# Kernel tuning notes

Hardware: AMD Instinct MI355X
Metric: run time of the kernel (lower is better)

The kernel has to match this reference:

```python
import jax, jax.numpy as jnp
import numpy as np
from jax import lax

B, L, F, D_MODEL = 4, 256, 80, 2048
ED, N, DT_RANK, K, NL = 4096, 16, 2, 4, 6  # d_inner, d_state, dt_rank, d_conv, n_layers


def setup_inputs():
    key = jax.random.key(0)
    ks = jax.random.split(key, 12)
    rn = lambda k, shp, s=0.02: jax.random.normal(k, shp, dtype=jnp.float32) * s
    return {
        "x": jax.random.normal(ks[0], (B, F, L), dtype=jnp.float32),
        "W_emb": rn(ks[1], (F, D_MODEL)),
        "b_emb": jnp.zeros((D_MODEL,), jnp.float32),
        "norm_w": jnp.ones((NL, D_MODEL), jnp.float32),
        "W_in": rn(ks[2], (NL, D_MODEL, 2 * ED)),
        "b_in": jnp.zeros((NL, 2 * ED), jnp.float32),
        "conv_w": rn(ks[3], (NL, ED, K), 0.1),
        "conv_b": jnp.zeros((NL, ED), jnp.float32),
        "W_x": rn(ks[4], (NL, ED, DT_RANK + 2 * N)),
        "W_dt": rn(ks[5], (NL, DT_RANK, ED), 0.1),
        "b_dt": jnp.full((NL, ED), -4.0, jnp.float32),
        "A_log": jnp.tile(jnp.log(jnp.arange(1, N + 1, dtype=jnp.float32))[None, None, :], (NL, ED, 1)),
        "Dp": jnp.ones((NL, ED), jnp.float32),
        "W_out": rn(ks[6], (NL, ED, D_MODEL)),
        "b_out": jnp.zeros((NL, D_MODEL), jnp.float32),
        "W_f": rn(ks[7], (D_MODEL, 1024)),
        "b_f": jnp.zeros((1024,), jnp.float32),
        "W_h1": rn(ks[8], (1024, 512), 0.05),
        "b_h1": jnp.zeros((512,), jnp.float32),
        "W_h2": rn(ks[9], (512, 256), 0.05),
        "b_h2": jnp.zeros((256,), jnp.float32),
        "W_h3": rn(ks[10], (256, 1), 0.05),
        "b_h3": jnp.zeros((1,), jnp.float32),
    }


def _rmsnorm(x, w, eps=1e-5):
    return x * lax.rsqrt(jnp.mean(x * x, axis=-1, keepdims=True) + eps) * w


def _mamba_block(u, W_in, b_in, conv_w, conv_b, W_x, W_dt, b_dt, A_log, Dp, W_out, b_out):
    xz = u @ W_in + b_in                        # (B,L,2*ED)
    xp, z = jnp.split(xz, 2, axis=-1)
    # causal depthwise conv over time, kernel K
    xc = lax.conv_general_dilated(
        xp.transpose(0, 2, 1), conv_w[:, None, :],
        window_strides=(1,), padding=[(K - 1, 0)],
        feature_group_count=ED,
        dimension_numbers=("NCH", "OIH", "NCH")).transpose(0, 2, 1) + conv_b
    xa = jax.nn.silu(xc)                        # (B,L,ED)
    dbc = xa @ W_x                              # (B,L,dt_rank+2N)
    dt = jax.nn.softplus(dbc[..., :DT_RANK] @ W_dt + b_dt)   # (B,L,ED)
    Bm = dbc[..., DT_RANK:DT_RANK + N]
    Cm = dbc[..., DT_RANK + N:]
    A = -jnp.exp(A_log)                         # (ED,N), negative

    def step(h, inp):
        xa_t, dt_t, B_t, C_t = inp
        h = jnp.exp(dt_t[:, :, None] * A) * h + (dt_t * xa_t)[:, :, None] * B_t[:, None, :]
        return h, jnp.einsum("ben,bn->be", h, C_t)

    step = jax.checkpoint(step)
    h0 = jnp.zeros((xa.shape[0], ED, N), xa.dtype)
    _, ys = lax.scan(step, h0, (xa.transpose(1, 0, 2), dt.transpose(1, 0, 2),
                                Bm.transpose(1, 0, 2), Cm.transpose(1, 0, 2)))
    y = ys.transpose(1, 0, 2) + Dp * xa
    y = y * jax.nn.silu(z)
    return y @ W_out + b_out


def reference(x, W_emb, b_emb, norm_w, W_in, b_in, conv_w, conv_b, W_x, W_dt, b_dt, A_log, Dp, W_out, b_out, W_f, b_f, W_h1, b_h1, W_h2, b_h2, W_h3, b_h3):
    h = x.transpose(0, 2, 1) @ W_emb + b_emb    # (B,L,D_MODEL)
    for i in range(NL):
        h = h + _mamba_block(_rmsnorm(h, norm_w[i]), W_in[i], b_in[i], conv_w[i], conv_b[i],
                             W_x[i], W_dt[i], b_dt[i], A_log[i], Dp[i], W_out[i], b_out[i])
    f = h[:, -1] @ W_f + b_f                    # (B,1024)
    g = jax.nn.silu(f @ W_h1 + b_h1)
    g = g @ W_h2 + b_h2
    g = jnp.where(g > 0, g, 0.01 * g)           # LeakyReLU(0.01)
    return jax.nn.sigmoid(g @ W_h3 + b_h3)      # (B,1)
```

## Files before the change

kernel.cpp:

```cpp
#include <hip/hip_runtime.h>
#include <hip/hip_bf16.h>
#include <math.h>

#define D_MODEL 2048
#define EDIM    4096
#define NSTATE  16
#define LSEQ    256
#define BATCH   4
#define NLAYER  6
#define FDIM    80

typedef __attribute__((ext_vector_type(8))) short bf16x8;
typedef __attribute__((ext_vector_type(4))) float f32x4;

__device__ __forceinline__ float silu_f(float x) { return x / (1.f + __expf(-x)); }

__device__ __forceinline__ float softplus_f(float v) {
  return (v > 20.f) ? v : __logf(1.f + __expf(v));
}

__device__ __forceinline__ unsigned short f2bf(float f) {
  unsigned u = __float_as_uint(f);
  unsigned r = u + 0x7fffu + ((u >> 16) & 1u);
  return (unsigned short)(r >> 16);
}

__device__ __forceinline__ void gload_lds16(const void* g, void* l) {
  __builtin_amdgcn_global_load_lds(
      (const __attribute__((address_space(1))) unsigned int*)g,
      (__attribute__((address_space(3))) unsigned int*)l, 16, 0, 0);
}

__global__ __launch_bounds__(256) void embed_kernel(
    const float* __restrict__ x, const float* __restrict__ W,
    const float* __restrict__ bias, float* __restrict__ h)
{
  int col = blockIdx.x * 256 + threadIdx.x;
  int row = blockIdx.y;
  int b = row >> 8, l = row & 255;
  const float* xp = x + (size_t)b * FDIM * LSEQ + l;
  float acc = bias[col];
  #pragma unroll 8
  for (int f = 0; f < FDIM; ++f)
    acc = fmaf(xp[(size_t)f * LSEQ], W[(size_t)f * D_MODEL + col], acc);
  h[(size_t)row * D_MODEL + col] = acc;
}

__global__ __launch_bounds__(256) void rmsnorm_kernel(
    const float* __restrict__ h, const float* __restrict__ w, unsigned short* __restrict__ u)
{
  int row = blockIdx.x;
  const float* hr = h + (size_t)row * D_MODEL;
  float s = 0.f;
  for (int i = threadIdx.x; i < D_MODEL; i += 256) { float v = hr[i]; s = fmaf(v, v, s); }
  #pragma unroll
  for (int o = 32; o > 0; o >>= 1) s += __shfl_down(s, o);
  __shared__ float red[4];
  int lane = threadIdx.x & 63, wid = threadIdx.x >> 6;
  if (lane == 0) red[wid] = s;
  __syncthreads();
  float total = red[0] + red[1] + red[2] + red[3];
  float scale = rsqrtf(total * (1.f / D_MODEL) + 1e-5f);
  unsigned short* ur = u + (size_t)row * D_MODEL;
  for (int i = threadIdx.x; i < D_MODEL; i += 256) ur[i] = f2bf(hr[i] * scale * w[i]);
}

__global__ __launch_bounds__(256) void wtrans_kernel(
    const float* __restrict__ W, unsigned short* __restrict__ WT, int K, int N)
{
  __shared__ float t[64][65];
  const int k0 = blockIdx.y * 64, n0 = blockIdx.x * 64;
  const int tc = (threadIdx.x & 15) << 2;
  const int tr = threadIdx.x >> 4;
  #pragma unroll
  for (int i = 0; i < 4; ++i) {
    int r = tr + (i << 4);
    float4 v = *(const float4*)(W + (size_t)(k0 + r) * N + n0 + tc);
    t[r][tc + 0] = v.x; t[r][tc + 1] = v.y; t[r][tc + 2] = v.z; t[r][tc + 3] = v.w;
  }
  __syncthreads();
  #pragma unroll
  for (int i = 0; i < 4; ++i) {
    int rr = tr + (i << 4);
    ushort4 o;
    o.x = f2bf(t[tc + 0][rr]);
    o.y = f2bf(t[tc + 1][rr]);
    o.z = f2bf(t[tc + 2][rr]);
    o.w = f2bf(t[tc + 3][rr]);
    *(ushort4*)(WT + (size_t)(n0 + rr) * K + k0 + tc) = o;
  }
}

__global__ __launch_bounds__(256) void wxt_kernel(
    const float* __restrict__ Wx, float* __restrict__ WxT)
{
  const int e = blockIdx.x * 256 + threadIdx.x;
  const int j = blockIdx.y;
  const int l = blockIdx.z;
  WxT[((size_t)l * 34 + j) * EDIM + e] = Wx[(size_t)l * EDIM * 34 + (size_t)e * 34 + j];
}

template<int BN>
__global__ __launch_bounds__(256) void gemm_bf16(
    const unsigned short* __restrict__ A, int lda,
    const unsigned short* __restrict__ BT, int ldb,
    const float* __restrict__ bias,
    const float* resid, int ldr,
    float* __restrict__ C, int ldc, int K)
{
  constexpr int BM = 128;
  constexpr int FN = BN / 32;
  __shared__ unsigned short As[2][BM * 32];
  __shared__ unsigned short Bs[2][BN * 32];
  const int tid  = threadIdx.x;
  const int wave = tid >> 6;
  const int lane = tid & 63;

  const int nwg = gridDim.x * gridDim.y;
  const int cpx = nwg >> 3;
  int flat = blockIdx.y * gridDim.x + blockIdx.x;
  flat = (flat & 7) * cpx + (flat >> 3);
  const int bm = (flat / gridDim.x) * BM;
  const int bn = (flat % gridDim.x) * BN;

  const int wr = (wave >> 1) * 64;
  const int wc = (wave & 1) * (BN / 2);
  const int srow = lane >> 2;
  const int scol = (lane & 3) * 8;

  auto stage = [&](int buf, int k0) {
    #pragma unroll
    for (int i = 0; i < BM / 64; ++i) {
      int c = wave + i * 4;
      gload_lds16(A + (size_t)(bm + c * 16 + srow) * lda + k0 + scol, &As[buf][c * 512]);
    }
    #pragma unroll
    for (int i = 0; i < BN / 64; ++i) {
      int c = wave + i * 4;
      gload_lds16(BT + (size_t)(bn + c * 16 + srow) * ldb + k0 + scol, &Bs[buf][c * 512]);
    }
  };

  f32x4 acc[4][FN];
  #pragma unroll
  for (int m = 0; m < 4; ++m)
    #pragma unroll
    for (int n = 0; n < FN; ++n)
      acc[m][n] = (f32x4){0.f, 0.f, 0.f, 0.f};

  stage(0, 0);
  const int nk = K >> 5;
  for (int t = 0; t < nk; ++t) {
    const int cur = t & 1;
    __syncthreads();
    if (t + 1 < nk) stage(cur ^ 1, (t + 1) << 5);
    bf16x8 af[4], bfr[FN];
    #pragma unroll
    for (int m = 0; m < 4; ++m)
      af[m] = *(const bf16x8*)&As[cur][(wr + m * 16 + (lane & 15)) * 32 + (lane >> 4) * 8];
    #pragma unroll
    for (int n = 0; n < FN; ++n)
      bfr[n] = *(const bf16x8*)&Bs[cur][(wc + n * 16 + (lane & 15)) * 32 + (lane >> 4) * 8];
    #pragma unroll
    for (int m = 0; m < 4; ++m)
      #pragma unroll
      for (int n = 0; n < FN; ++n)
        acc[m][n] = __builtin_amdgcn_mfma_f32_16x16x32_bf16(af[m], bfr[n], acc[m][n], 0, 0, 0);
  }

  const int rbase = (lane >> 4) * 4;
  const int cbase = lane & 15;
  #pragma unroll
  for (int m = 0; m < 4; ++m) {
    #pragma unroll
    for (int n = 0; n < FN; ++n) {
      const int col = bn + wc + n * 16 + cbase;
      const float bv = bias[col];
      #pragma unroll
      for (int r = 0; r < 4; ++r) {
        const int row = bm + wr + m * 16 + rbase + r;
        float v = acc[m][n][r] + bv;
        if (resid) v += resid[(size_t)row * ldr + col];
        C[(size_t)row * ldc + col] = v;
      }
    }
  }
}

__global__ __launch_bounds__(256) void conv_dbc_kernel(
    const float* __restrict__ xz, const float* __restrict__ cw,
    const float* __restrict__ cb, const float* __restrict__ WxT,
    float* __restrict__ xa, float* __restrict__ dbc)
{
  const int row = blockIdx.x;
  const int l = row & (LSEQ - 1);
  const int tid = threadIdx.x;
  float a[16];
  const float* base_row = xz + (size_t)row * 8192;
  #pragma unroll
  for (int k = 0; k < 16; ++k) {
    const int e = k * 256 + tid;
    float4 w = *(const float4*)(cw + (size_t)e * 4);
    const float* base = base_row + e;
    float v = cb[e];
    v = fmaf(w.w, base[0], v);
    if (l >= 1) v = fmaf(w.z, base[-8192], v);
    if (l >= 2) v = fmaf(w.y, base[-2 * 8192], v);
    if (l >= 3) v = fmaf(w.x, base[-3 * 8192], v);
    v = silu_f(v);
    a[k] = v;
    xa[(size_t)row * EDIM + e] = v;
  }
  __shared__ float red[34][4];
  const int lane = tid & 63, wid = tid >> 6;
  #pragma unroll
  for (int j = 0; j < 34; ++j) {
    const float* wr = WxT + (size_t)j * EDIM + tid;
    float s = 0.f;
    #pragma unroll
    for (int k = 0; k < 16; ++k)
      s = fmaf(a[k], wr[k * 256], s);
    #pragma unroll
    for (int o = 32; o > 0; o >>= 1) s += __shfl_down(s, o);
    if (lane == 0) red[j][wid] = s;
  }
  __syncthreads();
  if (tid < 34)
    dbc[(size_t)row * 34 + tid] = red[tid][0] + red[tid][1] + red[tid][2] + red[tid][3];
}

struct ScanIn { float x[4], z[4], d0[4], d1[4], B0[4], B1[4], C0[4], C1[4]; };

__device__ __forceinline__ void scan_load(
    ScanIn& s, const float* xap, const float* zp, const float* dp, int t0, int g)
{
  #pragma unroll
  for (int u = 0; u < 4; ++u) {
    const int t = t0 + u;
    s.x[u] = xap[(size_t)t * EDIM];
    s.z[u] = zp[(size_t)t * 8192];
    const float* dr = dp + (size_t)t * 34;
    s.d0[u] = dr[0];           s.d1[u] = dr[1];
    s.B0[u] = dr[2 + 2 * g];   s.B1[u] = dr[3 + 2 * g];
    s.C0[u] = dr[18 + 2 * g];  s.C1[u] = dr[19 + 2 * g];
  }
}

__device__ __forceinline__ void scan_step(
    const ScanIn& s, float& h0, float& h1,
    float w0, float w1, float bde, float Aa0, float Aa1, float dpe,
    int g, unsigned short* yp, int t0)
{
  #pragma unroll
  for (int u = 0; u < 4; ++u) {
    float v = fmaf(s.d1[u], w1, fmaf(s.d0[u], w0, bde));
    float dta = softplus_f(v);
    float dtxa = dta * s.x[u];
    h0 = fmaf(__expf(dta * Aa0), h0, dtxa * s.B0[u]);
    h1 = fmaf(__expf(dta * Aa1), h1, dtxa * s.B1[u]);
    float part = fmaf(h0, s.C0[u], h1 * s.C1[u]);
    part += __shfl_xor(part, 8);
    part += __shfl_xor(part, 16);
    part += __shfl_xor(part, 32);
    if (g == 0) {
      float yv = fmaf(dpe, s.x[u], part);
      yp[(size_t)(t0 + u) * EDIM] = f2bf(yv * silu_f(s.z[u]));
    }
  }
}

__global__ __launch_bounds__(256) void scan_kernel(
    const float* __restrict__ xz, const float* __restrict__ xa,
    const float* __restrict__ dbc,
    const float* __restrict__ Wdt, const float* __restrict__ bdt,
    const float* __restrict__ Alog, const float* __restrict__ Dpp,
    unsigned short* __restrict__ ybf)
{
  const int b = blockIdx.x >> 7;
  const int chunk = blockIdx.x & 127;
  const int wave = threadIdx.x >> 6;
  const int lane = threadIdx.x & 63;
  const int ch = lane & 7;
  const int g = lane >> 3;
  const int e = chunk * 32 + wave * 8 + ch;

  const float w0 = Wdt[e], w1 = Wdt[EDIM + e], bde = bdt[e];
  const float Aa0 = -__expf(Alog[(size_t)e * 16 + g * 2]);
  const float Aa1 = -__expf(Alog[(size_t)e * 16 + g * 2 + 1]);
  const float dpe = Dpp[e];
  float h0 = 0.f, h1 = 0.f;

  const float* xap = xa + (size_t)(b << 8) * EDIM + e;
  const float* zp  = xz + (size_t)(b << 8) * 8192 + EDIM + e;
  const float* dp  = dbc + (size_t)(b << 8) * 34;
  unsigned short* yp = ybf + (size_t)(b << 8) * EDIM + e;

  ScanIn sa, sb;
  scan_load(sa, xap, zp, dp, 0, g);
  for (int t0 = 0; t0 < LSEQ; t0 += 8) {
    scan_load(sb, xap, zp, dp, t0 + 4, g);
    scan_step(sa, h0, h1, w0, w1, bde, Aa0, Aa1, dpe, g, yp, t0);
    if (t0 + 8 < LSEQ) scan_load(sa, xap, zp, dp, t0 + 8, g);
    scan_step(sb, h0, h1, w0, w1, bde, Aa0, Aa1, dpe, g, yp, t0 + 4);
  }
}

template<int KS>
__global__ __launch_bounds__(256) void head_gemm_part(
    const float* __restrict__ in, int in_stride,
    const float* __restrict__ W, int N,
    float* __restrict__ part)
{
  const int j = blockIdx.x * 256 + threadIdx.x;
  const int b = blockIdx.y;
  const int s = blockIdx.z;
  const int k0 = s * KS;
  __shared__ float sIn[KS];
  if (threadIdx.x < KS) sIn[threadIdx.x] = in[(size_t)b * in_stride + k0 + threadIdx.x];
  __syncthreads();
  float acc = 0.f;
  #pragma unroll 8
  for (int k = 0; k < KS; ++k)
    acc = fmaf(sIn[k], W[(size_t)(k0 + k) * N + j], acc);
  part[((size_t)s * gridDim.y + b) * N + j] = acc;
}

__global__ __launch_bounds__(256) void head_reduce(
    const float* __restrict__ part, const float* __restrict__ bias,
    float* __restrict__ outp, int N, int S, int act)
{
  const int j = blockIdx.x * 256 + threadIdx.x;
  const int b = blockIdx.y;
  const int B = gridDim.y;
  float acc = bias[j];
  for (int s = 0; s < S; ++s)
    acc += part[((size_t)s * B + b) * N + j];
  if (act == 1) acc = silu_f(acc);
  else if (act == 2) acc = (acc > 0.f) ? acc : 0.01f * acc;
  outp[(size_t)b * N + j] = acc;
}

__global__ __launch_bounds__(256) void head_final_kernel(
    const float* __restrict__ g2, const float* __restrict__ W,
    const float* __restrict__ bb, float* __restrict__ out)
{
  int b_idx = threadIdx.x >> 6;
  int lane = threadIdx.x & 63;
  float s = 0.f;
  #pragma unroll
  for (int i = 0; i < 4; ++i) {
    int k = lane + i * 64;
    s = fmaf(g2[b_idx * 256 + k], W[k], s);
  }
  #pragma unroll
  for (int o = 32; o > 0; o >>= 1) s += __shfl_down(s, o);
  if (lane == 0) out[b_idx] = 1.f / (1.f + __expf(-(s + bb[0])));
}

extern "C" void kernel_launch(void* const* d_in, const int* in_sizes, int n_in,
                              void* d_out, int out_size, void* d_ws, size_t ws_size,
                              hipStream_t stream)
{
  const float* x      = (const float*)d_in[0];
  const float* W_emb  = (const float*)d_in[1];
  const float* b_emb  = (const float*)d_in[2];
  const float* norm_w = (const float*)d_in[3];
  const float* W_in   = (const float*)d_in[4];
  const float* b_in   = (const float*)d_in[5];
  const float* conv_w = (const float*)d_in[6];
  const float* conv_b = (const float*)d_in[7];
  const float* W_x    = (const float*)d_in[8];
  const float* W_dt   = (const float*)d_in[9];
  const float* b_dt   = (const float*)d_in[10];
  const float* A_log  = (const float*)d_in[11];
  const float* Dp     = (const float*)d_in[12];
  const float* W_out  = (const float*)d_in[13];
  const float* b_out  = (const float*)d_in[14];
  const float* W_f    = (const float*)d_in[15];
  const float* b_f    = (const float*)d_in[16];
  const float* W_h1   = (const float*)d_in[17];
  const float* b_h1   = (const float*)d_in[18];
  const float* W_h2   = (const float*)d_in[19];
  const float* b_h2   = (const float*)d_in[20];
  const float* W_h3   = (const float*)d_in[21];
  const float* b_h3   = (const float*)d_in[22];
  float* out = (float*)d_out;

  char* ws = (char*)d_ws;
  float*          hA  = (float*)ws;                 ws += (size_t)1024 * 2048 * 4;
  float*          hB  = (float*)ws;                 ws += (size_t)1024 * 2048 * 4;
  unsigned short* ubf = (unsigned short*)ws;        ws += (size_t)1024 * 2048 * 2;
  float*          xz  = (float*)ws;                 ws += (size_t)1024 * 8192 * 4;
  float*          xa  = (float*)ws;                 ws += (size_t)1024 * 4096 * 4;
  float*          dbc = (float*)ws;                 ws += (size_t)1024 * 40 * 4;
  unsigned short* ybf = (unsigned short*)ws;        ws += (size_t)1024 * 4096 * 2;
  unsigned short* WT  = (unsigned short*)ws;        ws += (size_t)8192 * 2048 * 2;
  float*          WxT = (float*)ws;                 ws += (size_t)NLAYER * 34 * EDIM * 4;
  float*          part= (float*)ws;                 ws += (size_t)16 * 4 * 1024 * 4;
  float*          fb  = (float*)ws;                 ws += 4096 * 4;
  float*          g1b = (float*)ws;                 ws += 2048 * 4;
  float*          g2b = (float*)ws;                 ws += 1024 * 4;

  embed_kernel<<<dim3(D_MODEL / 256, 1024), 256, 0, stream>>>(x, W_emb, b_emb, hA);
  wxt_kernel<<<dim3(EDIM / 256, 34, NLAYER), 256, 0, stream>>>(W_x, WxT);

  float* hin = hA;
  float* hout = hB;
  for (int i = 0; i < NLAYER; ++i) {
    const float* Wi  = W_in  + (size_t)i * 2048 * 8192;
    const float* bi  = b_in  + (size_t)i * 8192;
    const float* cwi = conv_w + (size_t)i * 4096 * 4;
    const float* cbi = conv_b + (size_t)i * 4096;
    const float* Wdti= W_dt  + (size_t)i * 2 * 4096;
    const float* bdti= b_dt  + (size_t)i * 4096;
    const float* Ali = A_log + (size_t)i * 4096 * 16;
    const float* Dpi = Dp    + (size_t)i * 4096;
    const float* Woi = W_out + (size_t)i * 4096 * 2048;
    const float* boi = b_out + (size_t)i * 2048;
    const float* nwi = norm_w + (size_t)i * 2048;

    rmsnorm_kernel<<<1024, 256, 0, stream>>>(hin, nwi, ubf);
    wtrans_kernel<<<dim3(8192 / 64, 2048 / 64), 256, 0, stream>>>(Wi, WT, 2048, 8192);
    gemm_bf16<128><<<dim3(8192 / 128, 1024 / 128), 256, 0, stream>>>(
        ubf, 2048, WT, 2048, bi, nullptr, 0, xz, 8192, 2048);
    conv_dbc_kernel<<<1024, 256, 0, stream>>>(
        xz, cwi, cbi, WxT + (size_t)i * 34 * EDIM, xa, dbc);
    scan_kernel<<<512, 256, 0, stream>>>(xz, xa, dbc, Wdti, bdti, Ali, Dpi, ybf);
    wtrans_kernel<<<dim3(2048 / 64, 4096 / 64), 256, 0, stream>>>(Woi, WT, 4096, 2048);
    gemm_bf16<64><<<dim3(2048 / 64, 1024 / 128), 256, 0, stream>>>(
        ybf, 4096, WT, 4096, boi, hin, 2048, hout, 2048, 4096);
    float* tmp = hin; hin = hout; hout = tmp;
  }

  head_gemm_part<128><<<dim3(1024 / 256, BATCH, 16), 256, 0, stream>>>(
      hin + (size_t)255 * 2048, 256 * 2048, W_f, 1024, part);
  head_reduce<<<dim3(1024 / 256, BATCH), 256, 0, stream>>>(part, b_f, fb, 1024, 16, 0);
  head_gemm_part<128><<<dim3(512 / 256, BATCH, 8), 256, 0, stream>>>(
      fb, 1024, W_h1, 512, part);
  head_reduce<<<dim3(512 / 256, BATCH), 256, 0, stream>>>(part, b_h1, g1b, 512, 8, 1);
  head_gemm_part<128><<<dim3(256 / 256, BATCH, 4), 256, 0, stream>>>(
      g1b, 512, W_h2, 256, part);
  head_reduce<<<dim3(256 / 256, BATCH), 256, 0, stream>>>(part, b_h2, g2b, 256, 4, 2);
  head_final_kernel<<<1, 256, 0, stream>>>(g2b, W_h3, b_h3, out);
}
```

Before: 1.799 ms.

## Split conv and x_proj, compute x_proj with bf16 MFMA GEMM

The fused conv+dbc kernel, which did per-row FP32 dot products against the transposed W_x, is split into an elementwise conv+SiLU kernel that also writes a bf16 copy of xa, followed by the bf16 MFMA GEMM. W_x is pre-transposed into bf16 padded to 64 columns, and dbc gets a stride of 64. The GEMM launches only 8 workgroups (1x8 grid) with K=4096, so parallelism is very low. Rounding xa and W_x to bf16 also reduces the precision of dt, B and C.

```diff
diff --git a/kernel.cpp b/kernel.cpp
--- a/kernel.cpp
+++ b/kernel.cpp
@@ -91,20 +91,21 @@
   }
 }
 
-__global__ __launch_bounds__(256) void wxt_kernel(
-    const float* __restrict__ Wx, float* __restrict__ WxT)
+__global__ __launch_bounds__(256) void wxtb_kernel(
+    const float* __restrict__ Wx, unsigned short* __restrict__ WxTb)
 {
   const int e = blockIdx.x * 256 + threadIdx.x;
   const int j = blockIdx.y;
   const int l = blockIdx.z;
-  WxT[((size_t)l * 34 + j) * EDIM + e] = Wx[(size_t)l * EDIM * 34 + (size_t)e * 34 + j];
+  float v = (j < 34) ? Wx[(size_t)l * EDIM * 34 + (size_t)e * 34 + j] : 0.f;
+  WxTb[((size_t)l * 64 + j) * EDIM + e] = f2bf(v);
 }
 
 template<int BN>
 __global__ __launch_bounds__(256) void gemm_bf16(
     const unsigned short* __restrict__ A, int lda,
     const unsigned short* __restrict__ BT, int ldb,
-    const float* __restrict__ bias,
+    const float* bias,
     const float* resid, int ldr,
     float* __restrict__ C, int ldc, int K)
 {
@@ -175,7 +176,7 @@
     #pragma unroll
     for (int n = 0; n < FN; ++n) {
       const int col = bn + wc + n * 16 + cbase;
-      const float bv = bias[col];
+      const float bv = bias ? bias[col] : 0.f;
       #pragma unroll
       for (int r = 0; r < 4; ++r) {
         const int row = bm + wr + m * 16 + rbase + r;
@@ -187,46 +188,25 @@
   }
 }
 
-__global__ __launch_bounds__(256) void conv_dbc_kernel(
+__global__ __launch_bounds__(256) void conv_silu_kernel(
     const float* __restrict__ xz, const float* __restrict__ cw,
-    const float* __restrict__ cb, const float* __restrict__ WxT,
-    float* __restrict__ xa, float* __restrict__ dbc)
-{
-  const int row = blockIdx.x;
-  const int l = row & (LSEQ - 1);
-  const int tid = threadIdx.x;
-  float a[16];
-  const float* base_row = xz + (size_t)row * 8192;
-  #pragma unroll
-  for (int k = 0; k < 16; ++k) {
-    const int e = k * 256 + tid;
-    float4 w = *(const float4*)(cw + (size_t)e * 4);
-    const float* base = base_row + e;
-    float v = cb[e];
-    v = fmaf(w.w, base[0], v);
-    if (l >= 1) v = fmaf(w.z, base[-8192], v);
-    if (l >= 2) v = fmaf(w.y, base[-2 * 8192], v);
-    if (l >= 3) v = fmaf(w.x, base[-3 * 8192], v);
-    v = silu_f(v);
-    a[k] = v;
-    xa[(size_t)row * EDIM + e] = v;
-  }
-  __shared__ float red[34][4];
-  const int lane = tid & 63, wid = tid >> 6;
-  #pragma unroll
-  for (int j = 0; j < 34; ++j) {
-    const float* wr = WxT + (size_t)j * EDIM + tid;
-    float s = 0.f;
-    #pragma unroll
-    for (int k = 0; k < 16; ++k)
-      s = fmaf(a[k], wr[k * 256], s);
-    #pragma unroll
-    for (int o = 32; o > 0; o >>= 1) s += __shfl_down(s, o);
-    if (lane == 0) red[j][wid] = s;
-  }
-  __syncthreads();
-  if (tid < 34)
-    dbc[(size_t)row * 34 + tid] = red[tid][0] + red[tid][1] + red[tid][2] + red[tid][3];
+    const float* __restrict__ cb, float* __restrict__ xa,
+    unsigned short* __restrict__ xab)
+{
+  int idx = blockIdx.x * 256 + threadIdx.x;
+  int e = idx & (EDIM - 1);
+  int row = idx >> 12;
+  int l = row & (LSEQ - 1);
+  float4 w = *(const float4*)(cw + (size_t)e * 4);
+  const float* base = xz + (size_t)row * 8192 + e;
+  float v = cb[e];
+  v = fmaf(w.w, base[0], v);
+  if (l >= 1) v = fmaf(w.z, base[-8192], v);
+  if (l >= 2) v = fmaf(w.y, base[-2 * 8192], v);
+  if (l >= 3) v = fmaf(w.x, base[-3 * 8192], v);
+  v = silu_f(v);
+  xa[idx] = v;
+  xab[idx] = f2bf(v);
 }
 
 struct ScanIn { float x[4], z[4], d0[4], d1[4], B0[4], B1[4], C0[4], C1[4]; };
@@ -239,7 +219,7 @@
     const int t = t0 + u;
     s.x[u] = xap[(size_t)t * EDIM];
     s.z[u] = zp[(size_t)t * 8192];
-    const float* dr = dp + (size_t)t * 34;
+    const float* dr = dp + (size_t)t * 64;
     s.d0[u] = dr[0];           s.d1[u] = dr[1];
     s.B0[u] = dr[2 + 2 * g];   s.B1[u] = dr[3 + 2 * g];
     s.C0[u] = dr[18 + 2 * g];  s.C1[u] = dr[19 + 2 * g];
@@ -292,7 +272,7 @@
 
   const float* xap = xa + (size_t)(b << 8) * EDIM + e;
   const float* zp  = xz + (size_t)(b << 8) * 8192 + EDIM + e;
-  const float* dp  = dbc + (size_t)(b << 8) * 34;
+  const float* dp  = dbc + (size_t)(b << 8) * 64;
   unsigned short* yp = ybf + (size_t)(b << 8) * EDIM + e;
 
   ScanIn sa, sb;
@@ -392,17 +372,18 @@
   unsigned short* ubf = (unsigned short*)ws;        ws += (size_t)1024 * 2048 * 2;
   float*          xz  = (float*)ws;                 ws += (size_t)1024 * 8192 * 4;
   float*          xa  = (float*)ws;                 ws += (size_t)1024 * 4096 * 4;
-  float*          dbc = (float*)ws;                 ws += (size_t)1024 * 40 * 4;
+  unsigned short* xab = (unsigned short*)ws;        ws += (size_t)1024 * 4096 * 2;
+  float*          dbc = (float*)ws;                 ws += (size_t)1024 * 64 * 4;
   unsigned short* ybf = (unsigned short*)ws;        ws += (size_t)1024 * 4096 * 2;
   unsigned short* WT  = (unsigned short*)ws;        ws += (size_t)8192 * 2048 * 2;
-  float*          WxT = (float*)ws;                 ws += (size_t)NLAYER * 34 * EDIM * 4;
+  unsigned short* WxTb= (unsigned short*)ws;        ws += (size_t)NLAYER * 64 * EDIM * 2;
   float*          part= (float*)ws;                 ws += (size_t)16 * 4 * 1024 * 4;
   float*          fb  = (float*)ws;                 ws += 4096 * 4;
   float*          g1b = (float*)ws;                 ws += 2048 * 4;
   float*          g2b = (float*)ws;                 ws += 1024 * 4;
 
   embed_kernel<<<dim3(D_MODEL / 256, 1024), 256, 0, stream>>>(x, W_emb, b_emb, hA);
-  wxt_kernel<<<dim3(EDIM / 256, 34, NLAYER), 256, 0, stream>>>(W_x, WxT);
+  wxtb_kernel<<<dim3(EDIM / 256, 64, NLAYER), 256, 0, stream>>>(W_x, WxTb);
 
   float* hin = hA;
   float* hout = hB;
@@ -423,8 +404,9 @@
     wtrans_kernel<<<dim3(8192 / 64, 2048 / 64), 256, 0, stream>>>(Wi, WT, 2048, 8192);
     gemm_bf16<128><<<dim3(8192 / 128, 1024 / 128), 256, 0, stream>>>(
         ubf, 2048, WT, 2048, bi, nullptr, 0, xz, 8192, 2048);
-    conv_dbc_kernel<<<1024, 256, 0, stream>>>(
-        xz, cwi, cbi, WxT + (size_t)i * 34 * EDIM, xa, dbc);
+    conv_silu_kernel<<<(1024 * 4096) / 256, 256, 0, stream>>>(xz, cwi, cbi, xa, xab);
+    gemm_bf16<64><<<dim3(1, 1024 / 128), 256, 0, stream>>>(
+        xab, 4096, WxTb + (size_t)i * 64 * EDIM, 4096, nullptr, nullptr, 0, dbc, 64, 4096);
     scan_kernel<<<512, 256, 0, stream>>>(xz, xa, dbc, Wdti, bdti, Ali, Dpi, ybf);
     wtrans_kernel<<<dim3(2048 / 64, 4096 / 64), 256, 0, stream>>>(Woi, WT, 4096, 2048);
     gemm_bf16<64><<<dim3(2048 / 64, 1024 / 128), 256, 0, stream>>>(
```

After: 2.076 ms. 15.4% more time.

## Transpose scan inputs to time-major bf16 layout for vectorized scan loads

Applied to the files above, without the earlier changes.

The conv kernel now writes its activations as bf16 and dbc transposed per batch, and a new transpose kernel converts xa and z into time-contiguous bf16 arrays. The scan then loads 8 timesteps per vector load and processes 8-step groups instead of doing strided per-step scalar loads. This targets the scan's latency-bound strided memory accesses. It adds an extra transpose kernel and its global traffic, and it lowers the precision of x and z to bf16 inside the scan.

```diff
diff --git a/kernel.cpp b/kernel.cpp
--- a/kernel.cpp
+++ b/kernel.cpp
@@ -23,6 +23,10 @@
   unsigned u = __float_as_uint(f);
   unsigned r = u + 0x7fffu + ((u >> 16) & 1u);
   return (unsigned short)(r >> 16);
+}
+
+__device__ __forceinline__ float bf2f(unsigned short u) {
+  return __uint_as_float((unsigned)u << 16);
 }
 
 __device__ __forceinline__ void gload_lds16(const void* g, void* l) {
@@ -104,7 +108,7 @@
 __global__ __launch_bounds__(256) void gemm_bf16(
     const unsigned short* __restrict__ A, int lda,
     const unsigned short* __restrict__ BT, int ldb,
-    const float* __restrict__ bias,
+    const float* bias,
     const float* resid, int ldr,
     float* __restrict__ C, int ldc, int K)
 {
@@ -175,7 +179,7 @@
     #pragma unroll
     for (int n = 0; n < FN; ++n) {
       const int col = bn + wc + n * 16 + cbase;
-      const float bv = bias[col];
+      const float bv = bias ? bias[col] : 0.f;
       #pragma unroll
       for (int r = 0; r < 4; ++r) {
         const int row = bm + wr + m * 16 + rbase + r;
@@ -190,10 +194,11 @@
 __global__ __launch_bounds__(256) void conv_dbc_kernel(
     const float* __restrict__ xz, const float* __restrict__ cw,
     const float* __restrict__ cb, const float* __restrict__ WxT,
-    float* __restrict__ xa, float* __restrict__ dbc)
+    unsigned short* __restrict__ xab, float* __restrict__ dbcT)
 {
   const int row = blockIdx.x;
   const int l = row & (LSEQ - 1);
+  const int b = row >> 8;
   const int tid = threadIdx.x;
   float a[16];
   const float* base_row = xz + (size_t)row * 8192;
@@ -209,7 +214,7 @@
     if (l >= 3) v = fmaf(w.x, base[-3 * 8192], v);
     v = silu_f(v);
     a[k] = v;
-    xa[(size_t)row * EDIM + e] = v;
+    xab[(size_t)row * EDIM + e] = f2bf(v);
   }
   __shared__ float red[34][4];
   const int lane = tid & 63, wid = tid >> 6;
@@ -226,33 +231,72 @@
   }
   __syncthreads();
   if (tid < 34)
-    dbc[(size_t)row * 34 + tid] = red[tid][0] + red[tid][1] + red[tid][2] + red[tid][3];
-}
-
-struct ScanIn { float x[4], z[4], d0[4], d1[4], B0[4], B1[4], C0[4], C1[4]; };
-
-__device__ __forceinline__ void scan_load(
-    ScanIn& s, const float* xap, const float* zp, const float* dp, int t0, int g)
-{
-  #pragma unroll
-  for (int u = 0; u < 4; ++u) {
-    const int t = t0 + u;
-    s.x[u] = xap[(size_t)t * EDIM];
-    s.z[u] = zp[(size_t)t * 8192];
-    const float* dr = dp + (size_t)t * 34;
-    s.d0[u] = dr[0];           s.d1[u] = dr[1];
-    s.B0[u] = dr[2 + 2 * g];   s.B1[u] = dr[3 + 2 * g];
-    s.C0[u] = dr[18 + 2 * g];  s.C1[u] = dr[19 + 2 * g];
-  }
-}
-
-__device__ __forceinline__ void scan_step(
-    const ScanIn& s, float& h0, float& h1,
+    dbcT[((size_t)b * 34 + tid) * 256 + l] =
+        red[tid][0] + red[tid][1] + red[tid][2] + red[tid][3];
+}
+
+__global__ __launch_bounds__(256) void tmajor_kernel(
+    const unsigned short* __restrict__ xab, const float* __restrict__ xz,
+    unsigned short* __restrict__ xT, unsigned short* __restrict__ zT)
+{
+  __shared__ unsigned short tx[64][72];
+  __shared__ unsigned short tz[64][72];
+  const int e0 = blockIdx.x * 64;
+  const int t0 = blockIdx.y * 64;
+  const int b  = blockIdx.z;
+  const int c  = threadIdx.x & 63;
+  const int r4 = threadIdx.x >> 6;
+  #pragma unroll
+  for (int i = 0; i < 16; ++i) {
+    int t = r4 + i * 4;
+    int row = (b << 8) + t0 + t;
+    tx[t][c] = xab[(size_t)row * EDIM + e0 + c];
+    tz[t][c] = f2bf(xz[(size_t)row * 8192 + EDIM + e0 + c]);
+  }
+  __syncthreads();
+  #pragma unroll
+  for (int i = 0; i < 16; ++i) {
+    int ee = r4 + i * 4;
+    xT[((size_t)b * EDIM + e0 + ee) * 256 + t0 + c] = tx[c][ee];
+    zT[((size_t)b * EDIM + e0 + ee) * 256 + t0 + c] = tz[c][ee];
+  }
+}
+
+struct ScanIn8 { float x[8], z[8], d0[8], d1[8], B0[8], B1[8], C0[8], C1[8]; };
+
+__device__ __forceinline__ void scan_load8(
+    ScanIn8& s, const unsigned short* xTp, const unsigned short* zTp,
+    const float* dp, int t0, int g)
+{
+  bf16x8 xv = *(const bf16x8*)&xTp[t0];
+  bf16x8 zv = *(const bf16x8*)&zTp[t0];
+  #pragma unroll
+  for (int u = 0; u < 8; ++u) {
+    s.x[u] = bf2f((unsigned short)xv[u]);
+    s.z[u] = bf2f((unsigned short)zv[u]);
+  }
+  const float* r;
+  r = dp + t0;                     *(float4*)&s.d0[0] = *(const float4*)&r[0];
+                                   *(float4*)&s.d0[4] = *(const float4*)&r[4];
+  r = dp + 256 + t0;               *(float4*)&s.d1[0] = *(const float4*)&r[0];
+                                   *(float4*)&s.d1[4] = *(const float4*)&r[4];
+  r = dp + (2 + 2 * g) * 256 + t0; *(float4*)&s.B0[0] = *(const float4*)&r[0];
+                                   *(float4*)&s.B0[4] = *(const float4*)&r[4];
+  r = dp + (3 + 2 * g) * 256 + t0; *(float4*)&s.B1[0] = *(const float4*)&r[0];
+                                   *(float4*)&s.B1[4] = *(const float4*)&r[4];
+  r = dp + (18 + 2 * g) * 256 + t0; *(float4*)&s.C0[0] = *(const float4*)&r[0];
+                                    *(float4*)&s.C0[4] = *(const float4*)&r[4];
+  r = dp + (19 + 2 * g) * 256 + t0; *(float4*)&s.C1[0] = *(const float4*)&r[0];
+                                    *(float4*)&s.C1[4] = *(const float4*)&r[4];
+}
+
+__device__ __forceinline__ void scan_step8(
+    const ScanIn8& s, float& h0, float& h1,
     float w0, float w1, float bde, float Aa0, float Aa1, float dpe,
     int g, unsigned short* yp, int t0)
 {
   #pragma unroll
-  for (int u = 0; u < 4; ++u) {
+  for (int u = 0; u < 8; ++u) {
     float v = fmaf(s.d1[u], w1, fmaf(s.d0[u], w0, bde));
     float dta = softplus_f(v);
     float dtxa = dta * s.x[u];
@@ -270,8 +314,8 @@
 }
 
 __global__ __launch_bounds__(256) void scan_kernel(
-    const float* __restrict__ xz, const float* __restrict__ xa,
-    const float* __restrict__ dbc,
+    const unsigned short* __restrict__ xT, const unsigned short* __restrict__ zT,
+    const float* __restrict__ dbcT,
     const float* __restrict__ Wdt, const float* __restrict__ bdt,
     const float* __restrict__ Alog, const float* __restrict__ Dpp,
     unsigned short* __restrict__ ybf)
@@ -290,18 +334,18 @@
   const float dpe = Dpp[e];
   float h0 = 0.f, h1 = 0.f;
 
-  const float* xap = xa + (size_t)(b << 8) * EDIM + e;
-  const float* zp  = xz + (size_t)(b << 8) * 8192 + EDIM + e;
-  const float* dp  = dbc + (size_t)(b << 8) * 34;
+  const unsigned short* xTp = xT + ((size_t)b * EDIM + e) * 256;
+  const unsigned short* zTp = zT + ((size_t)b * EDIM + e) * 256;
+  const float* dp = dbcT + (size_t)b * 34 * 256;
   unsigned short* yp = ybf + (size_t)(b << 8) * EDIM + e;
 
-  ScanIn sa, sb;
-  scan_load(sa, xap, zp, dp, 0, g);
-  for (int t0 = 0; t0 < LSEQ; t0 += 8) {
-    scan_load(sb, xap, zp, dp, t0 + 4, g);
-    scan_step(sa, h0, h1, w0, w1, bde, Aa0, Aa1, dpe, g, yp, t0);
-    if (t0 + 8 < LSEQ) scan_load(sa, xap, zp, dp, t0 + 8, g);
-    scan_step(sb, h0, h1, w0, w1, bde, Aa0, Aa1, dpe, g, yp, t0 + 4);
+  ScanIn8 sa, sb;
+  scan_load8(sa, xTp, zTp, dp, 0, g);
+  for (int t0 = 0; t0 < LSEQ; t0 += 16) {
+    scan_load8(sb, xTp, zTp, dp, t0 + 8, g);
+    scan_step8(sa, h0, h1, w0, w1, bde, Aa0, Aa1, dpe, g, yp, t0);
+    if (t0 + 16 < LSEQ) scan_load8(sa, xTp, zTp, dp, t0 + 16, g);
+    scan_step8(sb, h0, h1, w0, w1, bde, Aa0, Aa1, dpe, g, yp, t0 + 8);
   }
 }
 
@@ -391,8 +435,10 @@
   float*          hB  = (float*)ws;                 ws += (size_t)1024 * 2048 * 4;
   unsigned short* ubf = (unsigned short*)ws;        ws += (size_t)1024 * 2048 * 2;
   float*          xz  = (float*)ws;                 ws += (size_t)1024 * 8192 * 4;
-  float*          xa  = (float*)ws;                 ws += (size_t)1024 * 4096 * 4;
-  float*          dbc = (float*)ws;                 ws += (size_t)1024 * 40 * 4;
+  unsigned short* xab = (unsigned short*)ws;        ws += (size_t)1024 * 4096 * 2;
+  unsigned short* xT  = (unsigned short*)ws;        ws += (size_t)1024 * 4096 * 2;
+  unsigned short* zT  = (unsigned short*)ws;        ws += (size_t)1024 * 4096 * 2;
+  float*          dbcT= (float*)ws;                 ws += (size_t)4 * 34 * 256 * 4;
   unsigned short* ybf = (unsigned short*)ws;        ws += (size_t)1024 * 4096 * 2;
   unsigned short* WT  = (unsigned short*)ws;        ws += (size_t)8192 * 2048 * 2;
   float*          WxT = (float*)ws;                 ws += (size_t)NLAYER * 34 * EDIM * 4;
@@ -424,8 +470,9 @@
     gemm_bf16<128><<<dim3(8192 / 128, 1024 / 128), 256, 0, stream>>>(
         ubf, 2048, WT, 2048, bi, nullptr, 0, xz, 8192, 2048);
     conv_dbc_kernel<<<1024, 256, 0, stream>>>(
-        xz, cwi, cbi, WxT + (size_t)i * 34 * EDIM, xa, dbc);
-    scan_kernel<<<512, 256, 0, stream>>>(xz, xa, dbc, Wdti, bdti, Ali, Dpi, ybf);
+        xz, cwi, cbi, WxT + (size_t)i * 34 * EDIM, xab, dbcT);
+    tmajor_kernel<<<dim3(EDIM / 64, LSEQ / 64, BATCH), 256, 0, stream>>>(xab, xz, xT, zT);
+    scan_kernel<<<512, 256, 0, stream>>>(xT, zT, dbcT, Wdti, bdti, Ali, Dpi, ybf);
     wtrans_kernel<<<dim3(2048 / 64, 4096 / 64), 256, 0, stream>>>(Woi, WT, 4096, 2048);
     gemm_bf16<64><<<dim3(2048 / 64, 1024 / 128), 256, 0, stream>>>(
         ybf, 4096, WT, 4096, boi, hin, 2048, hout, 2048, 4096);
```

After: 1.841 ms. 1.02x slower.

## Stage scan inputs in LDS and store xa as bf16

Applied to the files above, without the earlier changes.

The conv kernel now writes its silu activation as bf16 instead of fp32, halving that buffer's traffic. The scan kernel bulk-loads its per-chunk x, z, dt and B/C slices for the whole sequence into shared memory with vectorized coalesced loads, storing most of it as bf16, then runs the recurrence from LDS. This replaces strided per-timestep global loads inside the sequential loop. It adds a bulk preload phase and lowers the precision of x, z, B and C inside the scan. The gemm bias argument also becomes nullable.

```diff
diff --git a/kernel.cpp b/kernel.cpp
--- a/kernel.cpp
+++ b/kernel.cpp
@@ -23,6 +23,10 @@
   unsigned u = __float_as_uint(f);
   unsigned r = u + 0x7fffu + ((u >> 16) & 1u);
   return (unsigned short)(r >> 16);
+}
+
+__device__ __forceinline__ float bf2f(unsigned short u) {
+  return __uint_as_float((unsigned)u << 16);
 }
 
 __device__ __forceinline__ void gload_lds16(const void* g, void* l) {
@@ -104,7 +108,7 @@
 __global__ __launch_bounds__(256) void gemm_bf16(
     const unsigned short* __restrict__ A, int lda,
     const unsigned short* __restrict__ BT, int ldb,
-    const float* __restrict__ bias,
+    const float* bias,
     const float* resid, int ldr,
     float* __restrict__ C, int ldc, int K)
 {
@@ -175,7 +179,7 @@
     #pragma unroll
     for (int n = 0; n < FN; ++n) {
       const int col = bn + wc + n * 16 + cbase;
-      const float bv = bias[col];
+      const float bv = bias ? bias[col] : 0.f;
       #pragma unroll
       for (int r = 0; r < 4; ++r) {
         const int row = bm + wr + m * 16 + rbase + r;
@@ -190,7 +194,7 @@
 __global__ __launch_bounds__(256) void conv_dbc_kernel(
     const float* __restrict__ xz, const float* __restrict__ cw,
     const float* __restrict__ cb, const float* __restrict__ WxT,
-    float* __restrict__ xa, float* __restrict__ dbc)
+    unsigned short* __restrict__ xab, float* __restrict__ dbc)
 {
   const int row = blockIdx.x;
   const int l = row & (LSEQ - 1);
@@ -209,7 +213,7 @@
     if (l >= 3) v = fmaf(w.x, base[-3 * 8192], v);
     v = silu_f(v);
     a[k] = v;
-    xa[(size_t)row * EDIM + e] = v;
+    xab[(size_t)row * EDIM + e] = f2bf(v);
   }
   __shared__ float red[34][4];
   const int lane = tid & 63, wid = tid >> 6;
@@ -230,21 +234,6 @@
 }
 
 struct ScanIn { float x[4], z[4], d0[4], d1[4], B0[4], B1[4], C0[4], C1[4]; };
-
-__device__ __forceinline__ void scan_load(
-    ScanIn& s, const float* xap, const float* zp, const float* dp, int t0, int g)
-{
-  #pragma unroll
-  for (int u = 0; u < 4; ++u) {
-    const int t = t0 + u;
-    s.x[u] = xap[(size_t)t * EDIM];
-    s.z[u] = zp[(size_t)t * 8192];
-    const float* dr = dp + (size_t)t * 34;
-    s.d0[u] = dr[0];           s.d1[u] = dr[1];
-    s.B0[u] = dr[2 + 2 * g];   s.B1[u] = dr[3 + 2 * g];
-    s.C0[u] = dr[18 + 2 * g];  s.C1[u] = dr[19 + 2 * g];
-  }
-}
 
 __device__ __forceinline__ void scan_step(
     const ScanIn& s, float& h0, float& h1,
@@ -270,37 +259,81 @@
 }
 
 __global__ __launch_bounds__(256) void scan_kernel(
-    const float* __restrict__ xz, const float* __restrict__ xa,
+    const unsigned short* __restrict__ xab, const float* __restrict__ xz,
     const float* __restrict__ dbc,
     const float* __restrict__ Wdt, const float* __restrict__ bdt,
     const float* __restrict__ Alog, const float* __restrict__ Dpp,
     unsigned short* __restrict__ ybf)
 {
+  __shared__ unsigned short sx[256 * 32];
+  __shared__ unsigned short sz[256 * 32];
+  __shared__ float          sd01[256 * 2];
+  __shared__ unsigned short sBC[256 * 32];
+
+  const int tid = threadIdx.x;
   const int b = blockIdx.x >> 7;
   const int chunk = blockIdx.x & 127;
-  const int wave = threadIdx.x >> 6;
-  const int lane = threadIdx.x & 63;
+  const int wave = tid >> 6;
+  const int lane = tid & 63;
   const int ch = lane & 7;
   const int g = lane >> 3;
-  const int e = chunk * 32 + wave * 8 + ch;
+  const int we = wave * 8 + ch;
+  const int e = chunk * 32 + we;
+
+  const unsigned short* xsrc = xab + (size_t)(b << 8) * EDIM + chunk * 32;
+  const float* zsrc = xz + (size_t)(b << 8) * 8192 + EDIM + chunk * 32;
+  const float* dsrc = dbc + (size_t)(b << 8) * 34;
+  #pragma unroll
+  for (int i = 0; i < 8; ++i) {
+    int idx = i * 256 + tid;
+    int t = idx >> 3, q = idx & 7;
+    *(ushort4*)&sx[t * 32 + q * 4] = *(const ushort4*)&xsrc[(size_t)t * EDIM + q * 4];
+    float4 v = *(const float4*)&zsrc[(size_t)t * 8192 + q * 4];
+    ushort4 o; o.x = f2bf(v.x); o.y = f2bf(v.y); o.z = f2bf(v.z); o.w = f2bf(v.w);
+    *(ushort4*)&sz[t * 32 + q * 4] = o;
+  }
+  {
+    float2 v = *(const float2*)&dsrc[(size_t)tid * 34];
+    *(float2*)&sd01[tid * 2] = v;
+  }
+  #pragma unroll
+  for (int i = 0; i < 16; ++i) {
+    int idx = i * 256 + tid;
+    int t = idx >> 4, q = idx & 15;
+    float2 v = *(const float2*)&dsrc[(size_t)t * 34 + 2 + q * 2];
+    ushort2 o; o.x = f2bf(v.x); o.y = f2bf(v.y);
+    *(ushort2*)&sBC[t * 32 + q * 2] = o;
+  }
+  __syncthreads();
 
   const float w0 = Wdt[e], w1 = Wdt[EDIM + e], bde = bdt[e];
   const float Aa0 = -__expf(Alog[(size_t)e * 16 + g * 2]);
   const float Aa1 = -__expf(Alog[(size_t)e * 16 + g * 2 + 1]);
   const float dpe = Dpp[e];
   float h0 = 0.f, h1 = 0.f;
-
-  const float* xap = xa + (size_t)(b << 8) * EDIM + e;
-  const float* zp  = xz + (size_t)(b << 8) * 8192 + EDIM + e;
-  const float* dp  = dbc + (size_t)(b << 8) * 34;
   unsigned short* yp = ybf + (size_t)(b << 8) * EDIM + e;
 
+  auto load = [&](ScanIn& s, int t0) {
+    #pragma unroll
+    for (int u = 0; u < 4; ++u) {
+      const int t = t0 + u;
+      s.x[u]  = bf2f(sx[t * 32 + we]);
+      s.z[u]  = bf2f(sz[t * 32 + we]);
+      s.d0[u] = sd01[t * 2];
+      s.d1[u] = sd01[t * 2 + 1];
+      s.B0[u] = bf2f(sBC[t * 32 + 2 * g]);
+      s.B1[u] = bf2f(sBC[t * 32 + 2 * g + 1]);
+      s.C0[u] = bf2f(sBC[t * 32 + 16 + 2 * g]);
+      s.C1[u] = bf2f(sBC[t * 32 + 16 + 2 * g + 1]);
+    }
+  };
+
   ScanIn sa, sb;
-  scan_load(sa, xap, zp, dp, 0, g);
+  load(sa, 0);
   for (int t0 = 0; t0 < LSEQ; t0 += 8) {
-    scan_load(sb, xap, zp, dp, t0 + 4, g);
+    load(sb, t0 + 4);
     scan_step(sa, h0, h1, w0, w1, bde, Aa0, Aa1, dpe, g, yp, t0);
-    if (t0 + 8 < LSEQ) scan_load(sa, xap, zp, dp, t0 + 8, g);
+    if (t0 + 8 < LSEQ) load(sa, t0 + 8);
     scan_step(sb, h0, h1, w0, w1, bde, Aa0, Aa1, dpe, g, yp, t0 + 4);
   }
 }
@@ -391,7 +424,7 @@
   float*          hB  = (float*)ws;                 ws += (size_t)1024 * 2048 * 4;
   unsigned short* ubf = (unsigned short*)ws;        ws += (size_t)1024 * 2048 * 2;
   float*          xz  = (float*)ws;                 ws += (size_t)1024 * 8192 * 4;
-  float*          xa  = (float*)ws;                 ws += (size_t)1024 * 4096 * 4;
+  unsigned short* xab = (unsigned short*)ws;        ws += (size_t)1024 * 4096 * 2;
   float*          dbc = (float*)ws;                 ws += (size_t)1024 * 40 * 4;
   unsigned short* ybf = (unsigned short*)ws;        ws += (size_t)1024 * 4096 * 2;
   unsigned short* WT  = (unsigned short*)ws;        ws += (size_t)8192 * 2048 * 2;
@@ -424,8 +457,8 @@
     gemm_bf16<128><<<dim3(8192 / 128, 1024 / 128), 256, 0, stream>>>(
         ubf, 2048, WT, 2048, bi, nullptr, 0, xz, 8192, 2048);
     conv_dbc_kernel<<<1024, 256, 0, stream>>>(
-        xz, cwi, cbi, WxT + (size_t)i * 34 * EDIM, xa, dbc);
-    scan_kernel<<<512, 256, 0, stream>>>(xz, xa, dbc, Wdti, bdti, Ali, Dpi, ybf);
+        xz, cwi, cbi, WxT + (size_t)i * 34 * EDIM, xab, dbc);
+    scan_kernel<<<512, 256, 0, stream>>>(xab, xz, dbc, Wdti, bdti, Ali, Dpi, ybf);
     wtrans_kernel<<<dim3(2048 / 64, 4096 / 64), 256, 0, stream>>>(Woi, WT, 4096, 2048);
     gemm_bf16<64><<<dim3(2048 / 64, 1024 / 128), 256, 0, stream>>>(
         ybf, 4096, WT, 4096, boi, hin, 2048, hout, 2048, 4096);
```

Result: no change. 1.783 ms (-0.9%).
